# Optimization experiments

Hardware: AMD Instinct MI355X
Metric: run time of the kernel (lower is better)

The kernel has to match this reference:

```python
import jax, jax.numpy as jnp
import numpy as np

B, T, C_IN, DIM, NFFT, HOP = 8, 1024, 256, 512, 1024, 256
NOUT = NFFT // 2 + 1
BB_DIL = (1, 1, 2, 2, 4, 4, 8, 8)
RES_DIL = (1, 3, 5)
N_RES = 3


def conv1d(x, w, b, dilation=1, groups=1, padding=0):
    # x: (B,C,T), w: (O, I/groups, K)
    y = jax.lax.conv_general_dilated(
        x, w, window_strides=(1,), padding=[(padding, padding)],
        rhs_dilation=(dilation,), dimension_numbers=('NCH', 'OIH', 'NCH'),
        feature_group_count=groups)
    return y + b[None, :, None]


def layernorm(x, g, b, eps=1e-6):
    m = jnp.mean(x, -1, keepdims=True)
    v = jnp.mean((x - m) ** 2, -1, keepdims=True)
    return (x - m) * jax.lax.rsqrt(v + eps) * g + b


def istft(spec, window):
    # spec: (B, F, Tf) complex, center=True, hann window, win_length=n_fft
    Bsz, F_, Tf = spec.shape
    frames = jnp.fft.irfft(spec, n=NFFT, axis=1)            # (B, n_fft, Tf)
    frames = jnp.transpose(frames, (0, 2, 1)) * window       # (B, Tf, n_fft)
    L = NFFT + HOP * (Tf - 1)
    idx = jnp.arange(Tf)[:, None] * HOP + jnp.arange(NFFT)[None, :]  # (Tf, n_fft)
    y = jnp.zeros((Bsz, L), frames.dtype).at[:, idx].add(frames)
    env = jnp.zeros((L,), window.dtype).at[idx].add(
        jnp.broadcast_to(window ** 2, (Tf, NFFT)))
    y = y / jnp.where(env > 1e-11, env, 1.0)
    start = NFFT // 2
    return y[:, start:start + HOP * (Tf - 1)]


def setup_inputs() -> dict:
    key = jax.random.key(0)
    ks = iter(jax.random.split(key, 64))
    r = lambda *s: jax.random.normal(next(ks), s, jnp.float32) * 0.02
    return {
        'x': jax.random.normal(next(ks), (B, T, C_IN), jnp.float32),
        'conv_in_w': r(DIM, C_IN, 7), 'conv_in_b': r(DIM),
        'skip_w': r(DIM, C_IN, 1), 'skip_b': r(DIM),
        'bb_dw_w': r(8, DIM, 1, 7), 'bb_dw_b': r(8, DIM),
        'bb_ln_g': jnp.ones((8, DIM), jnp.float32), 'bb_ln_b': jnp.zeros((8, DIM), jnp.float32),
        'bb_pw1_w': r(8, 4 * DIM, DIM), 'bb_pw1_b': r(8, 4 * DIM),
        'bb_pw2_w': r(8, DIM, 4 * DIM), 'bb_pw2_b': r(8, DIM),
        'bb_gamma': jnp.full((8, DIM), 1e-6, jnp.float32),
        'res_w1': r(N_RES, 3, DIM, DIM, 3), 'res_b1': r(N_RES, 3, DIM),
        'res_w2': r(N_RES, 3, DIM, DIM, 3), 'res_b2': r(N_RES, 3, DIM),
        'ln_g': jnp.ones((DIM,), jnp.float32), 'ln_b': jnp.zeros((DIM,), jnp.float32),
        'mag_w1': r(DIM, DIM), 'mag_b1': r(DIM),
        'mag_w2': r(NOUT, DIM), 'mag_b2': r(NOUT),
        'ph_w': r(NOUT, DIM), 'ph_b': r(NOUT),
        'cumsum_w': jnp.linspace(0.05, 0.4, NOUT, dtype=jnp.float32)[None, :],
        'window': (0.5 - 0.5 * jnp.cos(2.0 * jnp.pi * jnp.arange(NFFT) / NFFT)).astype(jnp.float32),
    }


def reference(x, conv_in_w, conv_in_b, skip_w, skip_b,
              bb_dw_w, bb_dw_b, bb_ln_g, bb_ln_b,
              bb_pw1_w, bb_pw1_b, bb_pw2_w, bb_pw2_b, bb_gamma,
              res_w1, res_b1, res_w2, res_b2,
              ln_g, ln_b, mag_w1, mag_b1, mag_w2, mag_b2,
              ph_w, ph_b, cumsum_w, window):
    # (B,T,C) -> (B,C,T)
    h = jnp.transpose(x, (0, 2, 1))
    skip = conv1d(h, skip_w, skip_b)                     # (B,DIM,T)
    hp = jnp.pad(h, ((0, 0), (0, 0), (3, 3)), mode='reflect')
    h = conv1d(hp, conv_in_w, conv_in_b)                 # kernel 7, pad 0 -> (B,DIM,T)
    # ConvNeXt backbone
    for i, d in enumerate(BB_DIL):
        res = h
        pad = (7 + (d - 1) * 6) // 2
        y = conv1d(h, bb_dw_w[i], bb_dw_b[i], dilation=d, groups=DIM, padding=pad)
        y = jnp.transpose(y, (0, 2, 1))                  # (B,T,DIM)
        y = layernorm(y, bb_ln_g[i], bb_ln_b[i])
        y = jax.nn.gelu(y @ bb_pw1_w[i].T + bb_pw1_b[i], approximate=False)
        y = y @ bb_pw2_w[i].T + bb_pw2_b[i]
        y = bb_gamma[i] * y
        h = res + jnp.transpose(y, (0, 2, 1))
    h = h + skip                                         # same length T
    # Residual dilated conv stacks
    for i in range(N_RES):
        for j, d in enumerate(RES_DIL):
            y = conv1d(h, res_w1[i, j], res_b1[i, j], dilation=d, padding=d)
            y = jax.nn.leaky_relu(y, 0.1)
            y = conv1d(y, res_w2[i, j], res_b2[i, j], padding=1)
            h = h + y
    h = jnp.transpose(h, (0, 2, 1))                      # (B,T,DIM)
    h = layernorm(h, ln_g, ln_b)
    # magnitude head
    m = jax.nn.gelu(h @ mag_w1.T + mag_b1, approximate=False)
    log_mag = m @ mag_w2.T + mag_b2
    mag = jnp.exp(jnp.clip(log_mag, -10.0, 10.0))        # (B,T,NOUT)
    # instantaneous-frequency phase head
    inst = jnp.tanh(h @ ph_w.T + ph_b) * jnp.pi
    phase = jnp.cumsum(inst * cumsum_w, axis=1)
    phase = jnp.remainder(phase + jnp.pi, 2.0 * jnp.pi) - jnp.pi
    # synthesize
    spec = jax.lax.complex(mag * jnp.cos(phase), mag * jnp.sin(phase))
    spec = jnp.transpose(spec, (0, 2, 1))                # (B,F,T)
    return istft(spec, window)
```

## Files before the change

kernel.cpp:

```cpp
#include <hip/hip_runtime.h>
#include <math.h>

constexpr int Bv = 8, Tv = 1024, DIMC = 512, NOUTC = 513;
constexpr int Mrows = Bv * 1024;
constexpr int LDS_S = 1056;
constexpr float PI_F = 3.14159265358979323846f;
constexpr float TWOPI_F = 6.28318530717958647692f;

struct TapInfo { int n; int off[7]; };
struct PtrTable { _Float16* h[36]; };

enum { BND_NONE = 0, BND_ZERO, BND_REFLECT };

typedef _Float16 half8v __attribute__((ext_vector_type(8)));
typedef _Float16 half4v __attribute__((ext_vector_type(4)));
typedef float f32x4 __attribute__((ext_vector_type(4)));

__device__ __forceinline__ void gld_lds16(const void* g, void* l) {
  __builtin_amdgcn_global_load_lds(
      (const __attribute__((address_space(1))) unsigned int*)g,
      (__attribute__((address_space(3))) unsigned int*)l, 16, 0, 0);
}

enum { MEPI_GELU_H = 0, MEPI_GAMMARES };

template<int EPI, int TN>
__global__ __launch_bounds__(256)
void mfma_gemm(const _Float16* __restrict__ A, int lda,
               const _Float16* __restrict__ W, int K,
               const float* __restrict__ bias,
               const float* __restrict__ aux,
               float* __restrict__ hio,
               _Float16* __restrict__ Ch,
               int N, int ldc)
{
  constexpr int NFR = TN / 32;
  __shared__ _Float16 sA[2][128 * 32];
  __shared__ _Float16 sB[2][TN * 32];
  const int m0 = blockIdx.x * 128;
  const int n0 = blockIdx.y * TN;
  const int tid = threadIdx.x;
  const int wid = tid >> 6, lane = tid & 63;
  const int wr = wid >> 1, wc = wid & 1;
  const int fr = lane & 15, fq = lane >> 4;

  f32x4 acc[4][NFR] = {};

  const int rbase = tid >> 2;
  const int kwS = (((tid & 3) ^ ((tid >> 3) & 3)) << 3);
  const int nkc = K >> 5;
  const int fqS = fq ^ ((fr >> 1) & 3);
  const int aBase = (wr * 64 + fr) * 32 + fqS * 8;
  const int bBase = (wc * (TN / 2) + fr) * 32 + fqS * 8;

  const _Float16* arow[2];
  #pragma unroll
  for (int s = 0; s < 2; ++s)
    arow[s] = A + (size_t)(m0 + s * 64 + rbase) * lda + kwS;

  auto STAGE = [&](int kc, int buf) {
    const int k0 = kc << 5;
    #pragma unroll
    for (int s = 0; s < 2; ++s)
      gld_lds16(arow[s] + k0, (char*)&sA[buf][0] + s * 4096 + wid * 1024);
    #pragma unroll
    for (int s = 0; s < TN / 64; ++s) {
      size_t bo = (size_t)(n0 + s * 64 + rbase) * K + kwS + k0;
      gld_lds16(W + bo, (char*)&sB[buf][0] + s * 4096 + wid * 1024);
    }
  };
  auto COMPUTE = [&](int buf) {
    half8v aF[4], bF[NFR];
    #pragma unroll
    for (int i = 0; i < 4; ++i) aF[i] = *(const half8v*)&sA[buf][aBase + i * 512];
    #pragma unroll
    for (int j = 0; j < NFR; ++j) bF[j] = *(const half8v*)&sB[buf][bBase + j * 512];
    #pragma unroll
    for (int i = 0; i < 4; ++i)
      #pragma unroll
      for (int j = 0; j < NFR; ++j)
        acc[i][j] = __builtin_amdgcn_mfma_f32_16x16x32_f16(aF[i], bF[j], acc[i][j], 0, 0, 0);
  };

  STAGE(0, 0);
  __syncthreads();
  int cur = 0;
  for (int kc = 0; kc < nkc; ++kc) {
    if (kc + 1 < nkc) STAGE(kc + 1, cur ^ 1);
    COMPUTE(cur);
    __syncthreads();
    cur ^= 1;
  }

  #pragma unroll
  for (int j = 0; j < NFR; ++j) {
    const int n = n0 + wc * (TN / 2) + j * 16 + fr;
    const float bj = bias[n];
    const float gj = (EPI == MEPI_GAMMARES) ? aux[n] : 0.f;
    #pragma unroll
    for (int i = 0; i < 4; ++i) {
      const int mB = m0 + wr * 64 + i * 16 + fq * 4;
      #pragma unroll
      for (int r = 0; r < 4; ++r) {
        const int m = mB + r;
        float v = acc[i][j][r] + bj;
        if (EPI == MEPI_GELU_H) {
          v = 0.5f * v * (1.f + erff(v * 0.70710678118654752f));
          Ch[(size_t)m * ldc + n] = (_Float16)v;
        } else {
          hio[(size_t)m * ldc + n] += gj * v;
        }
      }
    }
  }
}

enum { SEPI_F32 = 0, SEPI_LEAKY_SPLIT, SEPI_ADDRES_SPLIT,
       SEPI_GELU_SPLIT, SEPI_EXPCLIP, SEPI_TANHCW };

template<int EPI, int BND, int TN>
__global__ __launch_bounds__(256)
void mfma_gemm_split(const _Float16* __restrict__ Ah, const _Float16* __restrict__ Al, int lda,
                     const _Float16* __restrict__ Wh, const _Float16* __restrict__ Wl, int K,
                     const float* __restrict__ bias,
                     const float* __restrict__ aux,
                     float* __restrict__ hio,
                     float* __restrict__ Cf,
                     _Float16* __restrict__ Chh, _Float16* __restrict__ Chl,
                     int N, int ldc,
                     const _Float16* __restrict__ zpage,
                     TapInfo taps)
{
  constexpr int NFR = TN / 32;
  __shared__ _Float16 sAh[2][128 * 32];
  __shared__ _Float16 sAl[2][128 * 32];
  __shared__ _Float16 sBh[2][TN * 32];
  __shared__ _Float16 sBl[2][TN * 32];
  const int m0 = blockIdx.x * 128;
  const int n0 = blockIdx.y * TN;
  const int tid = threadIdx.x;
  const int wid = tid >> 6, lane = tid & 63;
  const int wr = wid >> 1, wc = wid & 1;
  const int fr = lane & 15, fq = lane >> 4;

  f32x4 acc[4][NFR] = {};

  const int t0 = m0 & (Tv - 1);
  const int rbase = tid >> 2;
  const int kwS = (((tid & 3) ^ ((tid >> 3) & 3)) << 3);
  const int nkc = K >> 5;
  const int NT = taps.n * nkc;
  const int fqS = fq ^ ((fr >> 1) & 3);
  const int aBase = (wr * 64 + fr) * 32 + fqS * 8;
  const int bBase = (wc * (TN / 2) + fr) * 32 + fqS * 8;

  auto STAGE = [&](int st, int buf) {
    int tap = (taps.n == 1) ? 0 : (st / nkc);
    int kc = st - tap * nkc;
    const int k0 = kc << 5;
    const int off = (BND == BND_NONE) ? 0 : taps.off[tap];
    const _Float16* Wth = Wh + (size_t)tap * N * K;
    const _Float16* Wtl = Wl + (size_t)tap * N * K;
    #pragma unroll
    for (int s = 0; s < 2; ++s) {
      int t = t0 + s * 64 + rbase + off;
      bool valid = true;
      if (BND == BND_REFLECT) t = (t < 0) ? -t : (t >= Tv ? 2 * Tv - 2 - t : t);
      else if (BND == BND_ZERO) valid = (t >= 0) && (t < Tv);
      size_t ro = (size_t)(m0 - t0 + t) * lda + kwS + k0;
      const void* sh = valid ? (const void*)(Ah + ro) : (const void*)zpage;
      const void* sl = valid ? (const void*)(Al + ro) : (const void*)zpage;
      gld_lds16(sh, (char*)&sAh[buf][0] + s * 4096 + wid * 1024);
      gld_lds16(sl, (char*)&sAl[buf][0] + s * 4096 + wid * 1024);
    }
    #pragma unroll
    for (int s = 0; s < TN / 64; ++s) {
      size_t bo = (size_t)(n0 + s * 64 + rbase) * K + kwS + k0;
      gld_lds16(Wth + bo, (char*)&sBh[buf][0] + s * 4096 + wid * 1024);
      gld_lds16(Wtl + bo, (char*)&sBl[buf][0] + s * 4096 + wid * 1024);
    }
  };

  auto COMPUTE = [&](int buf) {
    half8v ah[4], al[4], bh[NFR], bl[NFR];
    #pragma unroll
    for (int i = 0; i < 4; ++i) {
      ah[i] = *(const half8v*)&sAh[buf][aBase + i * 512];
      al[i] = *(const half8v*)&sAl[buf][aBase + i * 512];
    }
    #pragma unroll
    for (int j = 0; j < NFR; ++j) {
      bh[j] = *(const half8v*)&sBh[buf][bBase + j * 512];
      bl[j] = *(const half8v*)&sBl[buf][bBase + j * 512];
    }
    #pragma unroll
    for (int i = 0; i < 4; ++i)
      #pragma unroll
      for (int j = 0; j < NFR; ++j) {
        acc[i][j] = __builtin_amdgcn_mfma_f32_16x16x32_f16(ah[i], bh[j], acc[i][j], 0, 0, 0);
        acc[i][j] = __builtin_amdgcn_mfma_f32_16x16x32_f16(ah[i], bl[j], acc[i][j], 0, 0, 0);
        acc[i][j] = __builtin_amdgcn_mfma_f32_16x16x32_f16(al[i], bh[j], acc[i][j], 0, 0, 0);
      }
  };

  STAGE(0, 0);
  __syncthreads();
  int cur = 0;
  for (int st = 0; st < NT; ++st) {
    if (st + 1 < NT) STAGE(st + 1, cur ^ 1);
    COMPUTE(cur);
    __syncthreads();
    cur ^= 1;
  }

  #pragma unroll
  for (int j = 0; j < NFR; ++j) {
    const int n = n0 + wc * (TN / 2) + j * 16 + fr;
    const bool nok = (n < N);
    const float bj = (nok && bias) ? bias[n] : 0.f;
    const float ax = (EPI == SEPI_TANHCW && nok) ? aux[n] : 0.f;
    #pragma unroll
    for (int i = 0; i < 4; ++i) {
      const int mB = m0 + wr * 64 + i * 16 + fq * 4;
      #pragma unroll
      for (int r = 0; r < 4; ++r) {
        const int m = mB + r;
        float v = acc[i][j][r] + bj;
        if (!nok) continue;
        if (EPI == SEPI_F32) {
          Cf[(size_t)m * ldc + n] = v;
        } else if (EPI == SEPI_GELU_SPLIT) {
          v = 0.5f * v * (1.f + erff(v * 0.70710678118654752f));
          _Float16 hi = (_Float16)v;
          Chh[(size_t)m * ldc + n] = hi;
          Chl[(size_t)m * ldc + n] = (_Float16)(v - (float)hi);
        } else if (EPI == SEPI_EXPCLIP) {
          Cf[(size_t)m * ldc + n] = expf(fminf(fmaxf(v, -10.f), 10.f));
        } else if (EPI == SEPI_TANHCW) {
          Cf[(size_t)m * ldc + n] = tanhf(v) * PI_F * ax;
        }
      }
    }
  }
}

enum { REPI_LEAKY = 0, REPI_ADDRES };

template<int EPI>
__global__ __launch_bounds__(256)
void res_gemm(const _Float16* __restrict__ Ah, const _Float16* __restrict__ Al,
              const _Float16* __restrict__ Wh, const _Float16* __restrict__ Wl,
              const float* __restrict__ bias,
              float* __restrict__ hio,
              _Float16* __restrict__ Chh, _Float16* __restrict__ Chl,
              const _Float16* __restrict__ zpage,
              int d)
{
  __shared__ _Float16 sAh_[160 * 32];
  __shared__ _Float16 sAl_[160 * 32];
  __shared__ _Float16 sB_[3 * 2 * 64 * 32];
  const int m0 = blockIdx.x * 128;
  const int n0 = blockIdx.y * 64;
  const int tid = threadIdx.x;
  const int wid = tid >> 6, lane = tid & 63;
  const int wr = wid >> 1, wc = wid & 1;
  const int fr = lane & 15, fq = lane >> 4;
  const int t0 = m0 & (Tv - 1);

  f32x4 acc[4][2] = {};
  const int offs[3] = {-d, 0, d};

  for (int kc = 0; kc < 16; ++kc) {
    const int k0h = kc << 5;
    #pragma unroll
    for (int it = 0; it < 5; ++it) {
      int cb = it * 4 + wid;
      int half = (cb >= 10) ? 1 : 0;
      int rb = (cb - half * 10) * 16;
      int row = rb + (lane >> 2);
      int slot_g = (lane & 3) ^ ((row >> 1) & 3);
      int t = t0 - 16 + row;
      bool valid = (t >= 0) && (t < Tv);
      const _Float16* srcb = half ? Al : Ah;
      const void* src = valid
          ? (const void*)(srcb + (size_t)(m0 - t0 + t) * DIMC + k0h + slot_g * 8)
          : (const void*)(zpage + slot_g * 8);
      void* dst = (char*)(half ? sAl_ : sAh_) + rb * 64;
      gld_lds16(src, dst);
    }
    #pragma unroll
    for (int it = 0; it < 6; ++it) {
      int cb = it * 4 + wid;
      int tap = cb >> 3;
      int r2 = cb & 7;
      int half = r2 >> 2;
      int rb = (r2 & 3) * 16;
      int row = rb + (lane >> 2);
      int slot_g = (lane & 3) ^ ((row >> 1) & 3);
      const _Float16* srcb = (half ? Wl : Wh) + (size_t)tap * 512 * 512
                           + (size_t)(n0 + row) * 512 + k0h + slot_g * 8;
      void* dst = (char*)sB_ + ((size_t)(tap * 2 + half) * 64 + rb) * 64;
      gld_lds16(srcb, dst);
    }
    __syncthreads();

    #pragma unroll
    for (int tap = 0; tap < 3; ++tap) {
      const int off = offs[tap];
      half8v ah[4], al[4], bh[2], bl[2];
      #pragma unroll
      for (int i = 0; i < 4; ++i) {
        int rA = wr * 64 + i * 16 + fr + off + 16;
        int ab = rA * 64 + ((fq ^ ((rA >> 1) & 3)) * 16);
        ah[i] = *(const half8v*)((const char*)sAh_ + ab);
        al[i] = *(const half8v*)((const char*)sAl_ + ab);
      }
      #pragma unroll
      for (int j = 0; j < 2; ++j) {
        int rB = wc * 32 + j * 16 + fr;
        int bb = rB * 64 + ((fq ^ ((rB >> 1) & 3)) * 16);
        bh[j] = *(const half8v*)((const char*)sB_ + (tap * 2 + 0) * 4096 + bb);
        bl[j] = *(const half8v*)((const char*)sB_ + (tap * 2 + 1) * 4096 + bb);
      }
      #pragma unroll
      for (int i = 0; i < 4; ++i)
        #pragma unroll
        for (int j = 0; j < 2; ++j) {
          acc[i][j] = __builtin_amdgcn_mfma_f32_16x16x32_f16(ah[i], bh[j], acc[i][j], 0, 0, 0);
          acc[i][j] = __builtin_amdgcn_mfma_f32_16x16x32_f16(ah[i], bl[j], acc[i][j], 0, 0, 0);
          acc[i][j] = __builtin_amdgcn_mfma_f32_16x16x32_f16(al[i], bh[j], acc[i][j], 0, 0, 0);
        }
    }
    __syncthreads();
  }

  #pragma unroll
  for (int j = 0; j < 2; ++j) {
    const int n = n0 + wc * 32 + j * 16 + fr;
    const float bj = bias[n];
    #pragma unroll
    for (int i = 0; i < 4; ++i) {
      const int mB = m0 + wr * 64 + i * 16 + fq * 4;
      #pragma unroll
      for (int r = 0; r < 4; ++r) {
        const int m = mB + r;
        float v = acc[i][j][r] + bj;
        if (EPI == REPI_LEAKY) {
          v = (v > 0.f) ? v : 0.1f * v;
          _Float16 hi = (_Float16)v;
          Chh[(size_t)m * DIMC + n] = hi;
          Chl[(size_t)m * DIMC + n] = (_Float16)(v - (float)hi);
        } else {
          float nh = hio[(size_t)m * DIMC + n] + v;
          hio[(size_t)m * DIMC + n] = nh;
          _Float16 hi = (_Float16)nh;
          Chh[(size_t)m * DIMC + n] = hi;
          Chl[(size_t)m * DIMC + n] = (_Float16)(nh - (float)hi);
        }
      }
    }
  }
}

__global__ __launch_bounds__(256)
void dwln(const float* __restrict__ h, const float* __restrict__ w,
          const float* __restrict__ bias, const float* __restrict__ g,
          const float* __restrict__ be, _Float16* __restrict__ out, int d)
{
  int wid = threadIdx.x >> 6, lane = threadIdx.x & 63;
  int m = (blockIdx.x << 2) + wid;
  int t = m & (Tv - 1);
  int bT = m - t;
  float acc[8];
  #pragma unroll
  for (int q = 0; q < 8; ++q) {
    int c = lane + (q << 6);
    float s = bias[c];
    #pragma unroll
    for (int k = 0; k < 7; ++k) {
      int tt = t + (k - 3) * d;
      if (tt >= 0 && tt < Tv) s = fmaf(h[(size_t)(bT + tt) * DIMC + c], w[c * 7 + k], s);
    }
    acc[q] = s;
  }
  float sum = 0.f;
  #pragma unroll
  for (int q = 0; q < 8; ++q) sum += acc[q];
  #pragma unroll
  for (int o = 32; o > 0; o >>= 1) sum += __shfl_xor(sum, o);
  float mean = sum * (1.f / 512.f);
  float vs = 0.f;
  #pragma unroll
  for (int q = 0; q < 8; ++q) { float dd = acc[q] - mean; vs = fmaf(dd, dd, vs); }
  #pragma unroll
  for (int o = 32; o > 0; o >>= 1) vs += __shfl_xor(vs, o);
  float rstd = rsqrtf(vs * (1.f / 512.f) + 1e-6f);
  #pragma unroll
  for (int q = 0; q < 8; ++q) {
    int c = lane + (q << 6);
    out[(size_t)m * DIMC + c] = (_Float16)((acc[q] - mean) * rstd * g[c] + be[c]);
  }
}

__global__ __launch_bounds__(256)
void lnorm_split(const float* __restrict__ in, const float* __restrict__ g,
                 const float* __restrict__ be,
                 _Float16* __restrict__ ohi, _Float16* __restrict__ olo)
{
  int wid = threadIdx.x >> 6, lane = threadIdx.x & 63;
  int m = (blockIdx.x << 2) + wid;
  const float* row = in + (size_t)m * DIMC;
  float acc[8];
  #pragma unroll
  for (int q = 0; q < 8; ++q) acc[q] = row[lane + (q << 6)];
  float sum = 0.f;
  #pragma unroll
  for (int q = 0; q < 8; ++q) sum += acc[q];
  #pragma unroll
  for (int o = 32; o > 0; o >>= 1) sum += __shfl_xor(sum, o);
  float mean = sum * (1.f / 512.f);
  float vs = 0.f;
  #pragma unroll
  for (int q = 0; q < 8; ++q) { float dd = acc[q] - mean; vs = fmaf(dd, dd, vs); }
  #pragma unroll
  for (int o = 32; o > 0; o >>= 1) vs += __shfl_xor(vs, o);
  float rstd = rsqrtf(vs * (1.f / 512.f) + 1e-6f);
  #pragma unroll
  for (int q = 0; q < 8; ++q) {
    int c = lane + (q << 6);
    float v = (acc[q] - mean) * rstd * g[c] + be[c];
    _Float16 hi = (_Float16)v;
    ohi[(size_t)m * DIMC + c] = hi;
    olo[(size_t)m * DIMC + c] = (_Float16)(v - (float)hi);
  }
}

__global__ __launch_bounds__(256)
void add_split(float* __restrict__ a, const float* __restrict__ b,
               _Float16* __restrict__ hi, _Float16* __restrict__ lo, int n)
{
  int i = (blockIdx.x * 256 + threadIdx.x) * 4;
  if (i >= n) return;
  float4 va = *(const float4*)&a[i];
  float4 vb = *(const float4*)&b[i];
  float v[4] = {va.x + vb.x, va.y + vb.y, va.z + vb.z, va.w + vb.w};
  *(float4*)&a[i] = make_float4(v[0], v[1], v[2], v[3]);
  half4v h, l;
  #pragma unroll
  for (int q = 0; q < 4; ++q) {
    _Float16 hh = (_Float16)v[q];
    h[q] = hh; l[q] = (_Float16)(v[q] - (float)hh);
  }
  *(half4v*)&hi[i] = h;
  *(half4v*)&lo[i] = l;
}

__global__ __launch_bounds__(256)
void cvt_split(const float* __restrict__ in, _Float16* __restrict__ hi,
               _Float16* __restrict__ lo, int n)
{
  int i = (blockIdx.x * 256 + threadIdx.x) * 4;
  if (i >= n) return;
  float4 vv = *(const float4*)&in[i];
  float v[4] = {vv.x, vv.y, vv.z, vv.w};
  half4v h, l;
  #pragma unroll
  for (int q = 0; q < 4; ++q) {
    _Float16 hh = (_Float16)v[q];
    h[q] = hh; l[q] = (_Float16)(v[q] - (float)hh);
  }
  *(half4v*)&hi[i] = h;
  *(half4v*)&lo[i] = l;
}

__global__ __launch_bounds__(256)
void cvt_split_pad(const float* __restrict__ in, _Float16* __restrict__ hi,
                   _Float16* __restrict__ lo, int rows, int cols, int padRows)
{
  int i = blockIdx.x * 256 + threadIdx.x;
  if (i >= padRows * cols) return;
  int r = i / cols;
  float v = (r < rows) ? in[i] : 0.f;
  _Float16 h = (_Float16)v;
  hi[i] = h; lo[i] = (_Float16)(v - (float)h);
}

__global__ __launch_bounds__(256)
void cvt_h(const float* __restrict__ in, _Float16* __restrict__ out, int n)
{
  int i = (blockIdx.x * 256 + threadIdx.x) * 4;
  if (i >= n) return;
  float4 v = *(const float4*)&in[i];
  half4v h;
  h[0] = (_Float16)v.x; h[1] = (_Float16)v.y;
  h[2] = (_Float16)v.z; h[3] = (_Float16)v.w;
  *(half4v*)&out[i] = h;
}

__global__ __launch_bounds__(256)
void repack_split(const float* __restrict__ in, _Float16* __restrict__ hi,
                  _Float16* __restrict__ lo, int O, int C, int KT)
{
  int idx = blockIdx.x * 256 + threadIdx.x;
  if (idx >= O * C) return;
  int o = idx / C, c = idx - o * C;
  for (int k = 0; k < KT; ++k) {
    float v = in[((size_t)o * C + c) * KT + k];
    _Float16 h = (_Float16)v;
    size_t dst = ((size_t)k * O + o) * C + c;
    hi[dst] = h; lo[dst] = (_Float16)(v - (float)h);
  }
}

__global__ __launch_bounds__(256)
void repack_all(const float* __restrict__ res_w1, const float* __restrict__ res_w2,
                PtrTable pt)
{
  int blk = blockIdx.x;
  int conv = blk >> 10;
  int idx = ((blk & 1023) << 8) + threadIdx.x;
  int o = idx >> 9, c = idx & 511;
  const float* src = (conv < 9) ? (res_w1 + (size_t)conv * 786432)
                                : (res_w2 + (size_t)(conv - 9) * 786432);
  _Float16* hi = pt.h[conv * 2];
  _Float16* lo = pt.h[conv * 2 + 1];
  #pragma unroll
  for (int k = 0; k < 3; ++k) {
    float v = src[((size_t)o * 512 + c) * 3 + k];
    _Float16 hh = (_Float16)v;
    size_t dst = ((size_t)k * 512 + o) * 512 + c;
    hi[dst] = hh; lo[dst] = (_Float16)(v - (float)hh);
  }
}

__global__ __launch_bounds__(256)
void zero_fill16(_Float16* __restrict__ p)
{
  int i = threadIdx.x * 8;
  #pragma unroll
  for (int q = 0; q < 8; ++q) p[i + q] = (_Float16)0.f;
}

__global__ __launch_bounds__(256)
void build_basis_split(const float* __restrict__ window,
                       _Float16* __restrict__ bhi, _Float16* __restrict__ blo)
{
  int n = blockIdx.x;
  float wn = window[n];
  const float invN = 1.f / 1024.f;
  for (int j = threadIdx.x; j < LDS_S; j += 256) {
    float coef = 0.f;
    if (j < 513) {
      int k = j;
      if (k == 0)        coef = invN;
      else if (k == 512) coef = (n & 1) ? -invN : invN;
      else {
        int r = (k * n) & 1023;
        coef = 2.f * invN * cosf(TWOPI_F * (float)r * (1.f / 1024.f));
      }
    } else if (j < 1026) {
      int k = j - 513;
      if (k != 0 && k != 512) {
        int r = (k * n) & 1023;
        coef = -2.f * invN * sinf(TWOPI_F * (float)r * (1.f / 1024.f));
      }
    }
    float v = coef * wn;
    _Float16 hi = (_Float16)v;
    bhi[(size_t)n * LDS_S + j] = hi;
    blo[(size_t)n * LDS_S + j] = (_Float16)(v - (float)hi);
  }
}

__global__ __launch_bounds__(256)
void scan_part(const float* __restrict__ dph, float* __restrict__ psum)
{
  int b = blockIdx.x, fg = blockIdx.y;
  int w = threadIdx.x >> 6, lane = threadIdx.x & 63;
  int tc = blockIdx.z * 4 + w;
  int f = fg * 64 + lane;
  if (f >= NOUTC) return;
  const float* p = dph + (size_t)(b * Tv + tc * 32) * NOUTC + f;
  float s = 0.f;
  #pragma unroll 8
  for (int j = 0; j < 32; ++j) s += p[(size_t)j * NOUTC];
  psum[((size_t)b * 32 + tc) * 520 + f] = s;
}

__global__ __launch_bounds__(256)
void scan_off(float* __restrict__ psum)
{
  int idx = blockIdx.x * 256 + threadIdx.x;
  if (idx >= 8 * NOUTC) return;
  int b = idx / NOUTC, f = idx - b * NOUTC;
  float run = 0.f;
  for (int tc = 0; tc < 32; ++tc) {
    size_t o = ((size_t)b * 32 + tc) * 520 + f;
    float v = psum[o];
    psum[o] = run;
    run += v;
  }
}

__global__ __launch_bounds__(256)
void scan_emit(const float* __restrict__ dph, const float* __restrict__ mag,
               const float* __restrict__ psum,
               _Float16* __restrict__ Shi, _Float16* __restrict__ Slo)
{
  int b = blockIdx.x, fg = blockIdx.y;
  int w = threadIdx.x >> 6, lane = threadIdx.x & 63;
  int tc = blockIdx.z * 4 + w;
  int f = fg * 64 + lane;
  if (f >= NOUTC) return;
  float run = psum[((size_t)b * 32 + tc) * 520 + f];
  const size_t base = (size_t)(b * Tv + tc * 32) * NOUTC + f;
  for (int j = 0; j < 32; ++j) {
    run += dph[base + (size_t)j * NOUTC];
    float r = fmodf(run + PI_F, TWOPI_F);
    if (r < 0.f) r += TWOPI_F;
    float wph = r - PI_F;
    float mg = mag[base + (size_t)j * NOUTC];
    float sn, cs;
    sincosf(wph, &sn, &cs);
    size_t mrow = (size_t)(b * Tv + tc * 32 + j) * LDS_S;
    float vc = mg * cs, vs2 = mg * sn;
    _Float16 hc = (_Float16)vc, hs = (_Float16)vs2;
    Shi[mrow + f] = hc;        Slo[mrow + f] = (_Float16)(vc - (float)hc);
    Shi[mrow + 513 + f] = hs;  Slo[mrow + 513 + f] = (_Float16)(vs2 - (float)hs);
  }
}

__global__ __launch_bounds__(256)
void pad_S(_Float16* __restrict__ Shi, _Float16* __restrict__ Slo)
{
  int idx = blockIdx.x * 256 + threadIdx.x;
  if (idx >= Mrows * 30) return;
  int m = idx / 30, c = 1026 + idx % 30;
  Shi[(size_t)m * LDS_S + c] = (_Float16)0.f;
  Slo[(size_t)m * LDS_S + c] = (_Float16)0.f;
}

__global__ __launch_bounds__(256)
void ola(const float* __restrict__ frames, const float* __restrict__ window,
         float* __restrict__ out)
{
  int idx = blockIdx.x * 256 + threadIdx.x;
  if (idx >= Bv * 261888) return;
  int b = idx / 261888;
  int i = idx - b * 261888;
  int l = i + 512;
  int tmax = l >> 8; if (tmax > 1023) tmax = 1023;
  int tmin = (l >= 1023) ? ((l - 1023 + 255) >> 8) : 0;
  float acc = 0.f, env = 0.f;
  for (int t = tmin; t <= tmax; ++t) {
    int n = l - (t << 8);
    acc += frames[(size_t)(b * Tv + t) * 1024 + n];
    float wv = window[n];
    env = fmaf(wv, wv, env);
  }
  out[idx] = acc / (env > 1e-11f ? env : 1.f);
}

extern "C" void kernel_launch(void* const* d_in, const int* in_sizes, int n_in,
                              void* d_out, int out_size, void* d_ws, size_t ws_size,
                              hipStream_t stream)
{
  const float* x         = (const float*)d_in[0];
  const float* conv_in_w = (const float*)d_in[1];
  const float* conv_in_b = (const float*)d_in[2];
  const float* skip_w    = (const float*)d_in[3];
  const float* skip_b    = (const float*)d_in[4];
  const float* bb_dw_w   = (const float*)d_in[5];
  const float* bb_dw_b   = (const float*)d_in[6];
  const float* bb_ln_g   = (const float*)d_in[7];
  const float* bb_ln_b   = (const float*)d_in[8];
  const float* bb_pw1_w  = (const float*)d_in[9];
  const float* bb_pw1_b  = (const float*)d_in[10];
  const float* bb_pw2_w  = (const float*)d_in[11];
  const float* bb_pw2_b  = (const float*)d_in[12];
  const float* bb_gamma  = (const float*)d_in[13];
  const float* res_w1    = (const float*)d_in[14];
  const float* res_b1    = (const float*)d_in[15];
  const float* res_w2    = (const float*)d_in[16];
  const float* res_b2    = (const float*)d_in[17];
  const float* ln_g      = (const float*)d_in[18];
  const float* ln_b      = (const float*)d_in[19];
  const float* mag_w1    = (const float*)d_in[20];
  const float* mag_b1    = (const float*)d_in[21];
  const float* mag_w2    = (const float*)d_in[22];
  const float* mag_b2    = (const float*)d_in[23];
  const float* ph_w      = (const float*)d_in[24];
  const float* ph_b      = (const float*)d_in[25];
  const float* cumsum_w  = (const float*)d_in[26];
  const float* window    = (const float*)d_in[27];
  float* out = (float*)d_out;
  float* ws  = (float*)d_ws;

  float* w_h     = ws;
  float* w_skip  = ws + 4194304;
  float* w_t4    = ws + 8388608;
  float* w_mag   = ws + 12582912;
  float* w_dph   = ws + 16785408;
  float* w_basis = ws + 20987904;
  float* w_big   = ws + 22069248;
  _Float16* t3h  = (_Float16*)w_big;
  _Float16* h_hi = (_Float16*)w_big;
  _Float16* h_lo = h_hi + 4194304;
  _Float16* y_hi = h_hi + 8388608;
  _Float16* y_lo = h_hi + 12582912;
  _Float16* Shi  = (_Float16*)w_big;
  _Float16* Slo  = Shi + 8650752;
  float* w_frames= w_h;

  _Float16* t2h  = (_Float16*)(ws + 30720000);
  _Float16* x_hi = (_Float16*)(ws + 32817152);
  _Float16* x_lo = (_Float16*)(ws + 33865728);
  _Float16* wA_hi= (_Float16*)(ws + 34914304);
  _Float16* wA_lo= (_Float16*)(ws + 35438592);
  _Float16* wB_hi= (_Float16*)(ws + 35962880);
  _Float16* wB_lo= (_Float16*)(ws + 36487168);
  _Float16* zpg  = (_Float16*)(ws + 37011456);
  float* w_psum  = ws + 37012480;

  _Float16* wpw1h = (_Float16*)w_t4;
  _Float16* wpw2h = (_Float16*)w_mag;

  static const size_t slotOffF[18] = {
    8388608, 9175040, 9961472, 10747904, 11534336,
    12582912, 13369344, 14155776, 14942208, 15728640,
    16785408, 17571840, 18358272, 19144704, 19931136,
    32817152, 33603584,
    30720000
  };
  PtrTable pt;
  for (int cv = 0; cv < 18; ++cv) {
    _Float16* hi = (_Float16*)(ws + slotOffF[cv]);
    pt.h[cv * 2] = hi;
    pt.h[cv * 2 + 1] = hi + 786432;
  }

  _Float16* lshi = (_Float16*)w_skip;
  _Float16* lslo = lshi + 4194304;
  _Float16* t4hi = (_Float16*)w_t4;
  _Float16* t4lo = t4hi + 4194304;
  _Float16* m1hi = t2h;
  _Float16* m1lo = t2h + 262144;
  _Float16* m2hi = t2h + 524288;
  _Float16* m2lo = t2h + 851968;
  _Float16* phhi = t2h + 1179648;
  _Float16* phlo = t2h + 1507328;
  _Float16* bhi  = (_Float16*)w_basis;
  _Float16* blo  = bhi + 1081344;

  dim3 blk(256);
  TapInfo tp1{1, {0}};

  zero_fill16<<<dim3(1), blk, 0, stream>>>(zpg);
  cvt_split<<<dim3(8192 * 256 / 4 / 256), blk, 0, stream>>>(x, x_hi, x_lo, 8192 * 256);
  cvt_h<<<dim3(8388608 / 4 / 256), blk, 0, stream>>>(bb_pw1_w, wpw1h, 8388608);
  cvt_h<<<dim3(8388608 / 4 / 256), blk, 0, stream>>>(bb_pw2_w, wpw2h, 8388608);

  repack_split<<<dim3(512 * 256 / 256), blk, 0, stream>>>(conv_in_w, wA_hi, wA_lo, 512, 256, 7);
  {
    TapInfo tp{7, {-3, -2, -1, 0, 1, 2, 3}};
    mfma_gemm_split<SEPI_F32, BND_REFLECT, 64><<<dim3(64, 8), blk, 0, stream>>>(
        x_hi, x_lo, 256, wA_hi, wA_lo, 256, conv_in_b, nullptr, nullptr, w_h, nullptr, nullptr,
        512, 512, zpg, tp);
  }
  repack_split<<<dim3(512 * 256 / 256), blk, 0, stream>>>(skip_w, wB_hi, wB_lo, 512, 256, 1);
  mfma_gemm_split<SEPI_F32, BND_NONE, 64><<<dim3(64, 8), blk, 0, stream>>>(
      x_hi, x_lo, 256, wB_hi, wB_lo, 256, skip_b, nullptr, nullptr, w_skip, nullptr, nullptr,
      512, 512, zpg, tp1);

  const int dil[8] = {1, 1, 2, 2, 4, 4, 8, 8};
  for (int i = 0; i < 8; ++i) {
    dwln<<<dim3(2048), blk, 0, stream>>>(w_h, bb_dw_w + i * 512 * 7, bb_dw_b + i * 512,
                                         bb_ln_g + i * 512, bb_ln_b + i * 512, t2h, dil[i]);
    mfma_gemm<MEPI_GELU_H, 128><<<dim3(64, 16), blk, 0, stream>>>(
        t2h, 512, wpw1h + (size_t)i * 2048 * 512, 512, bb_pw1_b + i * 2048,
        nullptr, nullptr, t3h, 2048, 2048);
    mfma_gemm<MEPI_GAMMARES, 64><<<dim3(64, 8), blk, 0, stream>>>(
        t3h, 2048, wpw2h + (size_t)i * 512 * 2048, 2048, bb_pw2_b + i * 512,
        bb_gamma + i * 512, w_h, nullptr, 512, 512);
  }
  add_split<<<dim3(4194304 / 4 / 256), blk, 0, stream>>>(w_h, w_skip, h_hi, h_lo, 4194304);

  repack_all<<<dim3(18 * 1024), blk, 0, stream>>>(res_w1, res_w2, pt);

  const int rdil[3] = {1, 3, 5};
  for (int i = 0; i < 3; ++i)
    for (int j = 0; j < 3; ++j) {
      int d = rdil[j];
      int idx = i * 3 + j;
      res_gemm<REPI_LEAKY><<<dim3(64, 8), blk, 0, stream>>>(
          h_hi, h_lo, pt.h[idx * 2], pt.h[idx * 2 + 1],
          res_b1 + idx * 512, nullptr, y_hi, y_lo, zpg, d);
      res_gemm<REPI_ADDRES><<<dim3(64, 8), blk, 0, stream>>>(
          y_hi, y_lo, pt.h[(9 + idx) * 2], pt.h[(9 + idx) * 2 + 1],
          res_b2 + idx * 512, w_h, h_hi, h_lo, zpg, 1);
    }

  lnorm_split<<<dim3(2048), blk, 0, stream>>>(w_h, ln_g, ln_b, lshi, lslo);

  cvt_split<<<dim3(262144 / 4 / 256), blk, 0, stream>>>(mag_w1, m1hi, m1lo, 262144);
  cvt_split_pad<<<dim3(640 * 512 / 256), blk, 0, stream>>>(mag_w2, m2hi, m2lo, 513, 512, 640);
  cvt_split_pad<<<dim3(640 * 512 / 256), blk, 0, stream>>>(ph_w, phhi, phlo, 513, 512, 640);

  mfma_gemm_split<SEPI_GELU_SPLIT, BND_NONE, 64><<<dim3(64, 8), blk, 0, stream>>>(
      lshi, lslo, 512, m1hi, m1lo, 512, mag_b1, nullptr, nullptr, nullptr,
      t4hi, t4lo, 512, 512, zpg, tp1);
  mfma_gemm_split<SEPI_EXPCLIP, BND_NONE, 64><<<dim3(64, 10), blk, 0, stream>>>(
      t4hi, t4lo, 512, m2hi, m2lo, 512, mag_b2, nullptr, nullptr, w_mag,
      nullptr, nullptr, 513, 513, zpg, tp1);
  mfma_gemm_split<SEPI_TANHCW, BND_NONE, 64><<<dim3(64, 10), blk, 0, stream>>>(
      lshi, lslo, 512, phhi, phlo, 512, ph_b, cumsum_w, nullptr, w_dph,
      nullptr, nullptr, 513, 513, zpg, tp1);

  build_basis_split<<<dim3(1024), blk, 0, stream>>>(window, bhi, blo);
  pad_S<<<dim3((Mrows * 30 + 255) / 256), blk, 0, stream>>>(Shi, Slo);
  scan_part<<<dim3(8, 9, 8), blk, 0, stream>>>(w_dph, w_psum);
  scan_off<<<dim3(17), blk, 0, stream>>>(w_psum);
  scan_emit<<<dim3(8, 9, 8), blk, 0, stream>>>(w_dph, w_mag, w_psum, Shi, Slo);
  mfma_gemm_split<SEPI_F32, BND_NONE, 128><<<dim3(64, 8), blk, 0, stream>>>(
      Shi, Slo, LDS_S, bhi, blo, LDS_S, nullptr, nullptr, nullptr, w_frames,
      nullptr, nullptr, 1024, 1024, zpg, tp1);
  ola<<<dim3((Bv * 261888 + 255) / 256), blk, 0, stream>>>(w_frames, window, out);
}
```

Baseline: 1.976 ms.

## Add XCD-aware tile remap, dedicated conv-in GEMM with halo reuse, vectorize LN kernels

Remaps block indices so neighbouring tiles land on the same XCD, which should improve L2 sharing across all MFMA GEMMs. Replaces the generic 7-tap conv_in GEMM with a kernel that loads a 160-row halo of the input once per K chunk and reuses it across all taps, with reflect padding. Vectorizes the depthwise-conv+LN and layernorm-split kernels to use contiguous 8-channel float4/half8 accesses. The remap assumes the grid size is divisible by 8, and the conv_in kernel uses more LDS per block.

```diff
diff --git a/kernel.cpp b/kernel.cpp
--- a/kernel.cpp
+++ b/kernel.cpp
@@ -20,6 +20,14 @@
   __builtin_amdgcn_global_load_lds(
       (const __attribute__((address_space(1))) unsigned int*)g,
       (__attribute__((address_space(3))) unsigned int*)l, 16, 0, 0);
+}
+
+__device__ __forceinline__ void xcd_tile(int TMpix, int TNpix, int& m0, int& n0) {
+  const int lin = blockIdx.y * gridDim.x + blockIdx.x;
+  const int cpx = (gridDim.x * gridDim.y) >> 3;
+  const int nid = (lin & 7) * cpx + (lin >> 3);
+  m0 = (nid / gridDim.y) * TMpix;
+  n0 = (nid % gridDim.y) * TNpix;
 }
 
 enum { MEPI_GELU_H = 0, MEPI_GAMMARES };
@@ -37,8 +45,8 @@
   constexpr int NFR = TN / 32;
   __shared__ _Float16 sA[2][128 * 32];
   __shared__ _Float16 sB[2][TN * 32];
-  const int m0 = blockIdx.x * 128;
-  const int n0 = blockIdx.y * TN;
+  int m0, n0;
+  xcd_tile(128, TN, m0, n0);
   const int tid = threadIdx.x;
   const int wid = tid >> 6, lane = tid & 63;
   const int wr = wid >> 1, wc = wid & 1;
@@ -136,8 +144,8 @@
   __shared__ _Float16 sAl[2][128 * 32];
   __shared__ _Float16 sBh[2][TN * 32];
   __shared__ _Float16 sBl[2][TN * 32];
-  const int m0 = blockIdx.x * 128;
-  const int n0 = blockIdx.y * TN;
+  int m0, n0;
+  xcd_tile(128, TN, m0, n0);
   const int tid = threadIdx.x;
   const int wid = tid >> 6, lane = tid & 63;
   const int wr = wid >> 1, wc = wid & 1;
@@ -259,8 +267,8 @@
   __shared__ _Float16 sAh_[160 * 32];
   __shared__ _Float16 sAl_[160 * 32];
   __shared__ _Float16 sB_[3 * 2 * 64 * 32];
-  const int m0 = blockIdx.x * 128;
-  const int n0 = blockIdx.y * 64;
+  int m0, n0;
+  xcd_tile(128, 64, m0, n0);
   const int tid = threadIdx.x;
   const int wid = tid >> 6, lane = tid & 63;
   const int wr = wid >> 1, wc = wid & 1;
@@ -363,6 +371,103 @@
 }
 
 __global__ __launch_bounds__(256)
+void convin_gemm(const _Float16* __restrict__ Ah, const _Float16* __restrict__ Al,
+                 const _Float16* __restrict__ Wh, const _Float16* __restrict__ Wl,
+                 const float* __restrict__ bias,
+                 float* __restrict__ Cf)
+{
+  __shared__ _Float16 sAh_[160 * 32];
+  __shared__ _Float16 sAl_[160 * 32];
+  __shared__ _Float16 sB_[7 * 2 * 64 * 32];
+  int m0, n0;
+  xcd_tile(128, 64, m0, n0);
+  const int tid = threadIdx.x;
+  const int wid = tid >> 6, lane = tid & 63;
+  const int wr = wid >> 1, wc = wid & 1;
+  const int fr = lane & 15, fq = lane >> 4;
+  const int t0 = m0 & (Tv - 1);
+
+  f32x4 acc[4][2] = {};
+
+  for (int kc = 0; kc < 8; ++kc) {
+    const int k0h = kc << 5;
+    #pragma unroll
+    for (int it = 0; it < 5; ++it) {
+      int cb = it * 4 + wid;
+      int half = (cb >= 10) ? 1 : 0;
+      int rb = (cb - half * 10) * 16;
+      int row = rb + (lane >> 2);
+      int slot_g = (lane & 3) ^ ((row >> 1) & 3);
+      int t = t0 - 16 + row;
+      t = (t < 0) ? -t : (t >= Tv ? 2 * Tv - 2 - t : t);
+      const _Float16* srcb = half ? Al : Ah;
+      const void* src = srcb + (size_t)(m0 - t0 + t) * 256 + k0h + slot_g * 8;
+      void* dst = (char*)(half ? sAl_ : sAh_) + rb * 64;
+      gld_lds16(src, dst);
+    }
+    #pragma unroll
+    for (int it = 0; it < 14; ++it) {
+      int cb = it * 4 + wid;
+      int tap = cb >> 3;
+      int r2 = cb & 7;
+      int half = r2 >> 2;
+      int rb = (r2 & 3) * 16;
+      int row = rb + (lane >> 2);
+      int slot_g = (lane & 3) ^ ((row >> 1) & 3);
+      const _Float16* srcb = (half ? Wl : Wh) + (size_t)tap * 512 * 256
+                           + (size_t)(n0 + row) * 256 + k0h + slot_g * 8;
+      void* dst = (char*)sB_ + ((size_t)(tap * 2 + half) * 64 + rb) * 64;
+      gld_lds16(srcb, dst);
+    }
+    __syncthreads();
+
+    #pragma unroll
+    for (int tap = 0; tap < 7; ++tap) {
+      const int off = tap - 3;
+      half8v ah[4], al[4], bh[2], bl[2];
+      #pragma unroll
+      for (int i = 0; i < 4; ++i) {
+        int rA = wr * 64 + i * 16 + fr + off + 16;
+        int ab = rA * 64 + ((fq ^ ((rA >> 1) & 3)) * 16);
+        ah[i] = *(const half8v*)((const char*)sAh_ + ab);
+        al[i] = *(const half8v*)((const char*)sAl_ + ab);
+      }
+      #pragma unroll
+      for (int j = 0; j < 2; ++j) {
+        int rB = wc * 32 + j * 16 + fr;
+        int bb = rB * 64 + ((fq ^ ((rB >> 1) & 3)) * 16);
+        bh[j] = *(const half8v*)((const char*)sB_ + (tap * 2 + 0) * 4096 + bb);
+        bl[j] = *(const half8v*)((const char*)sB_ + (tap * 2 + 1) * 4096 + bb);
+      }
+      #pragma unroll
+      for (int i = 0; i < 4; ++i)
+        #pragma unroll
+        for (int j = 0; j < 2; ++j) {
+          acc[i][j] = __builtin_amdgcn_mfma_f32_16x16x32_f16(ah[i], bh[j], acc[i][j], 0, 0, 0);
+          acc[i][j] = __builtin_amdgcn_mfma_f32_16x16x32_f16(ah[i], bl[j], acc[i][j], 0, 0, 0);
+          acc[i][j] = __builtin_amdgcn_mfma_f32_16x16x32_f16(al[i], bh[j], acc[i][j], 0, 0, 0);
+        }
+    }
+    __syncthreads();
+  }
+
+  #pragma unroll
+  for (int j = 0; j < 2; ++j) {
+    const int n = n0 + wc * 32 + j * 16 + fr;
+    const float bj = bias[n];
+    #pragma unroll
+    for (int i = 0; i < 4; ++i) {
+      const int mB = m0 + wr * 64 + i * 16 + fq * 4;
+      #pragma unroll
+      for (int r = 0; r < 4; ++r) {
+        const int m = mB + r;
+        Cf[(size_t)m * DIMC + n] = acc[i][j][r] + bj;
+      }
+    }
+  }
+}
+
+__global__ __launch_bounds__(256)
 void dwln(const float* __restrict__ h, const float* __restrict__ w,
           const float* __restrict__ bias, const float* __restrict__ g,
           const float* __restrict__ be, _Float16* __restrict__ out, int d)
@@ -371,17 +476,25 @@
   int m = (blockIdx.x << 2) + wid;
   int t = m & (Tv - 1);
   int bT = m - t;
+  int c0 = lane * 8;
   float acc[8];
-  #pragma unroll
-  for (int q = 0; q < 8; ++q) {
-    int c = lane + (q << 6);
-    float s = bias[c];
-    #pragma unroll
-    for (int k = 0; k < 7; ++k) {
-      int tt = t + (k - 3) * d;
-      if (tt >= 0 && tt < Tv) s = fmaf(h[(size_t)(bT + tt) * DIMC + c], w[c * 7 + k], s);
-    }
-    acc[q] = s;
+  {
+    float4 b0 = *(const float4*)&bias[c0];
+    float4 b1 = *(const float4*)&bias[c0 + 4];
+    acc[0] = b0.x; acc[1] = b0.y; acc[2] = b0.z; acc[3] = b0.w;
+    acc[4] = b1.x; acc[5] = b1.y; acc[6] = b1.z; acc[7] = b1.w;
+  }
+  #pragma unroll
+  for (int k = 0; k < 7; ++k) {
+    int tt = t + (k - 3) * d;
+    if (tt < 0 || tt >= Tv) continue;
+    const float* hp = &h[(size_t)(bT + tt) * DIMC + c0];
+    float4 v0 = *(const float4*)hp;
+    float4 v1 = *(const float4*)(hp + 4);
+    float hv[8] = {v0.x, v0.y, v0.z, v0.w, v1.x, v1.y, v1.z, v1.w};
+    #pragma unroll
+    for (int q = 0; q < 8; ++q)
+      acc[q] = fmaf(hv[q], w[(c0 + q) * 7 + k], acc[q]);
   }
   float sum = 0.f;
   #pragma unroll
@@ -395,11 +508,17 @@
   #pragma unroll
   for (int o = 32; o > 0; o >>= 1) vs += __shfl_xor(vs, o);
   float rstd = rsqrtf(vs * (1.f / 512.f) + 1e-6f);
-  #pragma unroll
-  for (int q = 0; q < 8; ++q) {
-    int c = lane + (q << 6);
-    out[(size_t)m * DIMC + c] = (_Float16)((acc[q] - mean) * rstd * g[c] + be[c]);
-  }
+  float4 g0 = *(const float4*)&g[c0];
+  float4 g1 = *(const float4*)&g[c0 + 4];
+  float4 e0 = *(const float4*)&be[c0];
+  float4 e1 = *(const float4*)&be[c0 + 4];
+  float gv[8] = {g0.x, g0.y, g0.z, g0.w, g1.x, g1.y, g1.z, g1.w};
+  float ev[8] = {e0.x, e0.y, e0.z, e0.w, e1.x, e1.y, e1.z, e1.w};
+  half8v ov;
+  #pragma unroll
+  for (int q = 0; q < 8; ++q)
+    ov[q] = (_Float16)((acc[q] - mean) * rstd * gv[q] + ev[q]);
+  *(half8v*)&out[(size_t)m * DIMC + c0] = ov;
 }
 
 __global__ __launch_bounds__(256)
@@ -409,10 +528,11 @@
 {
   int wid = threadIdx.x >> 6, lane = threadIdx.x & 63;
   int m = (blockIdx.x << 2) + wid;
-  const float* row = in + (size_t)m * DIMC;
-  float acc[8];
-  #pragma unroll
-  for (int q = 0; q < 8; ++q) acc[q] = row[lane + (q << 6)];
+  int c0 = lane * 8;
+  const float* row = in + (size_t)m * DIMC + c0;
+  float4 v0 = *(const float4*)row;
+  float4 v1 = *(const float4*)(row + 4);
+  float acc[8] = {v0.x, v0.y, v0.z, v0.w, v1.x, v1.y, v1.z, v1.w};
   float sum = 0.f;
   #pragma unroll
   for (int q = 0; q < 8; ++q) sum += acc[q];
@@ -425,14 +545,21 @@
   #pragma unroll
   for (int o = 32; o > 0; o >>= 1) vs += __shfl_xor(vs, o);
   float rstd = rsqrtf(vs * (1.f / 512.f) + 1e-6f);
+  float4 g0 = *(const float4*)&g[c0];
+  float4 g1 = *(const float4*)&g[c0 + 4];
+  float4 e0 = *(const float4*)&be[c0];
+  float4 e1 = *(const float4*)&be[c0 + 4];
+  float gv[8] = {g0.x, g0.y, g0.z, g0.w, g1.x, g1.y, g1.z, g1.w};
+  float ev[8] = {e0.x, e0.y, e0.z, e0.w, e1.x, e1.y, e1.z, e1.w};
+  half8v hv, lv;
   #pragma unroll
   for (int q = 0; q < 8; ++q) {
-    int c = lane + (q << 6);
-    float v = (acc[q] - mean) * rstd * g[c] + be[c];
+    float v = (acc[q] - mean) * rstd * gv[q] + ev[q];
     _Float16 hi = (_Float16)v;
-    ohi[(size_t)m * DIMC + c] = hi;
-    olo[(size_t)m * DIMC + c] = (_Float16)(v - (float)hi);
-  }
+    hv[q] = hi; lv[q] = (_Float16)(v - (float)hi);
+  }
+  *(half8v*)&ohi[(size_t)m * DIMC + c0] = hv;
+  *(half8v*)&olo[(size_t)m * DIMC + c0] = lv;
 }
 
 __global__ __launch_bounds__(256)
@@ -761,12 +888,8 @@
   cvt_h<<<dim3(8388608 / 4 / 256), blk, 0, stream>>>(bb_pw2_w, wpw2h, 8388608);
 
   repack_split<<<dim3(512 * 256 / 256), blk, 0, stream>>>(conv_in_w, wA_hi, wA_lo, 512, 256, 7);
-  {
-    TapInfo tp{7, {-3, -2, -1, 0, 1, 2, 3}};
-    mfma_gemm_split<SEPI_F32, BND_REFLECT, 64><<<dim3(64, 8), blk, 0, stream>>>(
-        x_hi, x_lo, 256, wA_hi, wA_lo, 256, conv_in_b, nullptr, nullptr, w_h, nullptr, nullptr,
-        512, 512, zpg, tp);
-  }
+  convin_gemm<<<dim3(64, 8), blk, 0, stream>>>(
+      x_hi, x_lo, wA_hi, wA_lo, conv_in_b, w_h);
   repack_split<<<dim3(512 * 256 / 256), blk, 0, stream>>>(skip_w, wB_hi, wB_lo, 512, 256, 1);
   mfma_gemm_split<SEPI_F32, BND_NONE, 64><<<dim3(64, 8), blk, 0, stream>>>(
       x_hi, x_lo, 256, wB_hi, wB_lo, 256, skip_b, nullptr, nullptr, w_skip, nullptr, nullptr,
```

New measurement: 2.182 ms. 1.1x slower.
